# Optimization experiments

Hardware: AMD Instinct MI355X
Metric: run time of the kernel (lower is better)

## Reference

```python
import jax, jax.numpy as jnp
import numpy as np

def setup_inputs() -> dict:
    key = jax.random.key(0)
    inputs_embeds = jax.random.normal(key, (16, 8192, 256), dtype=jnp.float32)
    return {"inputs_embeds": inputs_embeds}

def reference(inputs_embeds):
    # cumulative prefix mean along seq dim: mean over [:i+1] = cumsum / (i+1)
    S = inputs_embeds.shape[1]
    csum = jnp.cumsum(inputs_embeds, axis=1)  # [B, S, D]
    denom = jnp.arange(1, S + 1, dtype=inputs_embeds.dtype)[None, :, None]
    return (csum / denom,)
```

## Files before the change

### kernel.cpp

```cpp
#include <hip/hip_runtime.h>

#define BB 16
#define SS 8192
#define DD 256
#define D4 (DD / 4)
#define NC 128
#define CL (SS / NC)

__global__ __launch_bounds__(64) void avgseq_chunksum(const float4* __restrict__ x,
                                                      float4* __restrict__ ws) {
    const int blk = blockIdx.x;
    const int b = blk >> 7;
    const int c = blk & (NC - 1);
    const int t = threadIdx.x;

    const float4* p = x + ((size_t)b * SS + (size_t)c * CL) * D4 + t;
    float4 acc = make_float4(0.f, 0.f, 0.f, 0.f);
#pragma unroll 8
    for (int s = 0; s < CL; ++s) {
        float4 v = p[(size_t)s * D4];
        acc.x += v.x; acc.y += v.y; acc.z += v.z; acc.w += v.w;
    }
    ws[((size_t)b * NC + c) * D4 + t] = acc;
}

__global__ __launch_bounds__(64) void avgseq_scan(const float4* __restrict__ x,
                                                  const float4* __restrict__ ws,
                                                  float4* __restrict__ out) {
    const int blk = blockIdx.x;
    const int b = blk >> 7;
    const int c = blk & (NC - 1);
    const int t = threadIdx.x;

    const float4* w = ws + (size_t)b * NC * D4 + t;
    float4 pre = make_float4(0.f, 0.f, 0.f, 0.f);
#pragma unroll 4
    for (int cc = 0; cc < c; ++cc) {
        float4 v = w[(size_t)cc * D4];
        pre.x += v.x; pre.y += v.y; pre.z += v.z; pre.w += v.w;
    }

    const size_t base = ((size_t)b * SS + (size_t)c * CL) * D4 + t;
    const float4* p = x + base;
    float4* o = out + base;
    const int s0 = c * CL;

    float4 acc = pre;
#pragma unroll 8
    for (int s = 0; s < CL; ++s) {
        float4 v = p[(size_t)s * D4];
        acc.x += v.x; acc.y += v.y; acc.z += v.z; acc.w += v.w;
        const float r = __builtin_amdgcn_rcpf((float)(s0 + s + 1));
        float4 ov = make_float4(acc.x * r, acc.y * r, acc.z * r, acc.w * r);
        o[(size_t)s * D4] = ov;
    }
}

extern "C" void kernel_launch(void* const* d_in, const int* in_sizes, int n_in,
                              void* d_out, int out_size, void* d_ws, size_t ws_size,
                              hipStream_t stream) {
    const float4* x = (const float4*)d_in[0];
    float4* out = (float4*)d_out;
    float4* ws = (float4*)d_ws;

    const int nblocks = BB * NC;
    avgseq_chunksum<<<nblocks, 64, 0, stream>>>(x, ws);
    avgseq_scan<<<nblocks, 64, 0, stream>>>(x, ws, out);
}
```

Measured before the change: 255.6 us.

## Add chunk-prefix scan kernel, double chunk count, batch loads in groups

Doubles the number of sequence chunks so more blocks run concurrently. A new small kernel turns the per-chunk sums into exclusive prefixes, which replaces the per-block serial loop over all earlier chunks in the scan kernel. Both main kernels now issue 16 loads back to back before accumulating, to keep more memory requests in flight. The cost is one extra launch whose 16 blocks do serial work, plus higher register use from the grouped loads.

Result: slower. 260.9 us (+2.1%).

```diff
diff --git a/kernel.cpp b/kernel.cpp
--- a/kernel.cpp
+++ b/kernel.cpp
@@ -4,55 +4,72 @@
 #define SS 8192
 #define DD 256
 #define D4 (DD / 4)
-#define NC 128
+#define NC 256
 #define CL (SS / NC)
+#define G  16
 
 __global__ __launch_bounds__(64) void avgseq_chunksum(const float4* __restrict__ x,
                                                       float4* __restrict__ ws) {
     const int blk = blockIdx.x;
-    const int b = blk >> 7;
+    const int b = blk >> 8;
     const int c = blk & (NC - 1);
     const int t = threadIdx.x;
 
     const float4* p = x + ((size_t)b * SS + (size_t)c * CL) * D4 + t;
     float4 acc = make_float4(0.f, 0.f, 0.f, 0.f);
-#pragma unroll 8
-    for (int s = 0; s < CL; ++s) {
-        float4 v = p[(size_t)s * D4];
-        acc.x += v.x; acc.y += v.y; acc.z += v.z; acc.w += v.w;
+    for (int s0 = 0; s0 < CL; s0 += G) {
+        float4 v[G];
+#pragma unroll
+        for (int g = 0; g < G; ++g) v[g] = p[(size_t)(s0 + g) * D4];
+#pragma unroll
+        for (int g = 0; g < G; ++g) {
+            acc.x += v[g].x; acc.y += v[g].y; acc.z += v[g].z; acc.w += v[g].w;
+        }
     }
     ws[((size_t)b * NC + c) * D4 + t] = acc;
+}
+
+__global__ __launch_bounds__(64) void avgseq_scanws(float4* __restrict__ ws) {
+    const int b = blockIdx.x;
+    const int t = threadIdx.x;
+    float4* w = ws + (size_t)b * NC * D4 + t;
+    float4 run = make_float4(0.f, 0.f, 0.f, 0.f);
+#pragma unroll 8
+    for (int c = 0; c < NC; ++c) {
+        float4 v = w[(size_t)c * D4];
+        w[(size_t)c * D4] = run;
+        run.x += v.x; run.y += v.y; run.z += v.z; run.w += v.w;
+    }
 }
 
 __global__ __launch_bounds__(64) void avgseq_scan(const float4* __restrict__ x,
                                                   const float4* __restrict__ ws,
                                                   float4* __restrict__ out) {
     const int blk = blockIdx.x;
-    const int b = blk >> 7;
+    const int b = blk >> 8;
     const int c = blk & (NC - 1);
     const int t = threadIdx.x;
 
-    const float4* w = ws + (size_t)b * NC * D4 + t;
-    float4 pre = make_float4(0.f, 0.f, 0.f, 0.f);
-#pragma unroll 4
-    for (int cc = 0; cc < c; ++cc) {
-        float4 v = w[(size_t)cc * D4];
-        pre.x += v.x; pre.y += v.y; pre.z += v.z; pre.w += v.w;
-    }
+    float4 acc = ws[((size_t)b * NC + c) * D4 + t];
 
     const size_t base = ((size_t)b * SS + (size_t)c * CL) * D4 + t;
     const float4* p = x + base;
     float4* o = out + base;
     const int s0 = c * CL;
 
-    float4 acc = pre;
-#pragma unroll 8
-    for (int s = 0; s < CL; ++s) {
-        float4 v = p[(size_t)s * D4];
-        acc.x += v.x; acc.y += v.y; acc.z += v.z; acc.w += v.w;
-        const float r = __builtin_amdgcn_rcpf((float)(s0 + s + 1));
-        float4 ov = make_float4(acc.x * r, acc.y * r, acc.z * r, acc.w * r);
-        o[(size_t)s * D4] = ov;
+    for (int ss = 0; ss < CL; ss += G) {
+        float4 v[G];
+#pragma unroll
+        for (int g = 0; g < G; ++g) v[g] = p[(size_t)(ss + g) * D4];
+        float4 ov[G];
+#pragma unroll
+        for (int g = 0; g < G; ++g) {
+            acc.x += v[g].x; acc.y += v[g].y; acc.z += v[g].z; acc.w += v[g].w;
+            const float r = __builtin_amdgcn_rcpf((float)(s0 + ss + g + 1));
+            ov[g] = make_float4(acc.x * r, acc.y * r, acc.z * r, acc.w * r);
+        }
+#pragma unroll
+        for (int g = 0; g < G; ++g) o[(size_t)(ss + g) * D4] = ov[g];
     }
 }
 
@@ -65,5 +82,6 @@
 
     const int nblocks = BB * NC;
     avgseq_chunksum<<<nblocks, 64, 0, stream>>>(x, ws);
+    avgseq_scanws<<<BB, 64, 0, stream>>>(ws);
     avgseq_scan<<<nblocks, 64, 0, stream>>>(x, ws, out);
 }
```
